# Kernel optimization log

Measured on AMD Instinct MI355X. Metric: run time of the kernel, lower is better.

Reference implementation:

```python
import jax, jax.numpy as jnp
import numpy as np

B, N, DIM = 4, 16384, 512
H, D, S = 8, 64, 64  # heads, dim_head, n_global_queries
SCALE = 1.0  # FLARE hardcodes scale=1.0


def setup_inputs() -> dict:
    key = jax.random.key(0)
    ks = jax.random.split(key, 10)
    inner = H * D
    s = 0.02
    return {
        "x": jax.random.normal(ks[0], (B, N, DIM), dtype=jnp.float32),
        "q_global": jax.random.normal(ks[1], (1, H, S, D), dtype=jnp.float32),
        "Wx": jax.random.normal(ks[2], (DIM, inner), dtype=jnp.float32) * s,
        "bx": jnp.zeros((inner,), dtype=jnp.float32),
        "Wk": jax.random.normal(ks[3], (D, D), dtype=jnp.float32) * s,
        "bk": jnp.zeros((D,), dtype=jnp.float32),
        "Wv": jax.random.normal(ks[4], (D, D), dtype=jnp.float32) * s,
        "bv": jnp.zeros((D,), dtype=jnp.float32),
        "Wo": jax.random.normal(ks[5], (inner, DIM), dtype=jnp.float32) * s,
        "bo": jnp.zeros((DIM,), dtype=jnp.float32),
    }


def reference(x, q_global, Wx, bx, Wk, bk, Wv, bv, Wo, bo):
    b, n, c = x.shape
    # input projection + split heads: B N (H D) -> B H N D
    x_mid = (x @ Wx + bx).reshape(b, n, H, D).transpose(0, 2, 1, 3)
    # per-head k/v projections (dim_head x dim_head)
    k = x_mid @ Wk + bk  # [B,H,N,D]
    v = x_mid @ Wv + bv  # [B,H,N,D]
    G = q_global  # broadcast over batch
    # pass 1: aggregate tokens into S global slots
    attn1 = jax.nn.softmax(jnp.einsum('bhsd,bhnd->bhsn', jnp.broadcast_to(G, (b, H, S, D)), k) * SCALE, axis=-1)
    z = jnp.einsum('bhsn,bhnd->bhsd', attn1, v)  # [B,H,S,D]
    # pass 2: distribute slots back to tokens (query=k, key=G, value=z)
    attn2 = jax.nn.softmax(jnp.einsum('bhnd,bhsd->bhns', k, jnp.broadcast_to(G, (b, H, S, D))) * SCALE, axis=-1)
    y = jnp.einsum('bhns,bhsd->bhnd', attn2, z)  # [B,H,N,D]
    # merge heads + output projection
    out = y.transpose(0, 2, 1, 3).reshape(b, n, H * D)
    return out @ Wo + bo
```

## Files before the change

### kernel.cpp

```cpp
#include <hip/hip_runtime.h>
#include <stdint.h>

#define DEV __device__ __forceinline__

typedef __attribute__((ext_vector_type(8))) short bf16x8;
typedef __attribute__((ext_vector_type(4))) float f32x4;
typedef __attribute__((ext_vector_type(8))) unsigned short u16x8;
typedef __attribute__((ext_vector_type(4))) unsigned short u16x4;

DEV unsigned short f2bf(float f) {
  union { float f; unsigned int u; } v; v.f = f;
  unsigned int u = v.u;
  return (unsigned short)((u + 0x7FFFu + ((u >> 16) & 1u)) >> 16);
}
DEV float bf2f(unsigned short u) {
  union { unsigned int u; float f; } v; v.u = ((unsigned int)u) << 16;
  return v.f;
}
DEV f32x4 mfma16(bf16x8 a, bf16x8 b, f32x4 c) {
  return __builtin_amdgcn_mfma_f32_16x16x32_bf16(a, b, c, 0, 0, 0);
}

__global__ __launch_bounds__(256) void k_cvt_bf16(const float* __restrict__ in,
                                                  unsigned short* __restrict__ out,
                                                  int n8) {
  int i = blockIdx.x * 256 + threadIdx.x;
  if (i >= n8) return;
  const float4* p = (const float4*)in + (size_t)i * 2;
  float4 a = p[0], b = p[1];
  u16x8 o;
  o[0] = f2bf(a.x); o[1] = f2bf(a.y); o[2] = f2bf(a.z); o[3] = f2bf(a.w);
  o[4] = f2bf(b.x); o[5] = f2bf(b.y); o[6] = f2bf(b.z); o[7] = f2bf(b.w);
  ((u16x8*)out)[i] = o;
}

__global__ void k_gk(const float* __restrict__ Wk, const float* __restrict__ qg,
                     float* __restrict__ GK) {
  int idx = blockIdx.x * 256 + threadIdx.x;
  int dd = idx & 63, hs = idx >> 6;
  float a = 0.f;
#pragma unroll 8
  for (int d = 0; d < 64; ++d) a += Wk[dd * 64 + d] * qg[(size_t)hs * 64 + d];
  GK[idx] = a;
}

__global__ void k_wl(const float* __restrict__ Wx, const float* __restrict__ GK,
                     unsigned short* __restrict__ Wcat) {
  int idx = blockIdx.x * 256 + threadIdx.x;
  int c = idx & 511, hs = idx >> 9;
  int h = hs >> 6;
  float a = 0.f;
#pragma unroll 8
  for (int dd = 0; dd < 64; ++dd) a += Wx[(size_t)c * 512 + h * 64 + dd] * GK[hs * 64 + dd];
  Wcat[(size_t)hs * 512 + c] = f2bf(a);
}

__global__ void k_wv(const float* __restrict__ Wx, const float* __restrict__ Wv,
                     unsigned short* __restrict__ Wcat) {
  int idx = blockIdx.x * 256 + threadIdx.x;
  int c = idx & 511, o = idx >> 9;
  int h = o >> 6, dp = o & 63;
  float a = 0.f;
#pragma unroll 8
  for (int dd = 0; dd < 64; ++dd) a += Wx[(size_t)c * 512 + h * 64 + dd] * Wv[dd * 64 + dp];
  Wcat[(size_t)(512 + o) * 512 + c] = f2bf(a);
}

__global__ void k_bias2(const float* __restrict__ bx, const float* __restrict__ bk,
                        const float* __restrict__ bv, const float* __restrict__ Wv,
                        const float* __restrict__ qg, const float* __restrict__ GK,
                        float* __restrict__ bias) {
  int o = blockIdx.x * 256 + threadIdx.x;
  if (o >= 1024) return;
  if (o < 512) {
    int h = o >> 6;
    float a = 0.f;
    for (int dd = 0; dd < 64; ++dd) a += bx[h * 64 + dd] * GK[(size_t)o * 64 + dd];
    for (int dp = 0; dp < 64; ++dp) a += bk[dp] * qg[(size_t)o * 64 + dp];
    bias[o] = a;
  } else {
    int o2 = o - 512, h = o2 >> 6, dp = o2 & 63;
    float a = bv[dp];
    for (int dd = 0; dd < 64; ++dd) a += bx[h * 64 + dd] * Wv[dd * 64 + dp];
    bias[o] = a;
  }
}

__global__ void k_wo_t(const float* __restrict__ Wo, unsigned short* __restrict__ WoT) {
  int idx = blockIdx.x * 256 + threadIdx.x;
  int i = idx >> 9, o = idx & 511;
  WoT[(size_t)o * 512 + i] = f2bf(Wo[(size_t)i * 512 + o]);
}

template <int MODE>
__global__ __launch_bounds__(512, 1) void k_mm2(const unsigned short* __restrict__ A,
                                                const unsigned short* __restrict__ Bsrc,
                                                const float* __restrict__ bias,
                                                unsigned short* __restrict__ P2,
                                                float* __restrict__ zpart,
                                                float* __restrict__ dpart,
                                                float* __restrict__ out) {
  extern __shared__ char lds[];
  const int tid = threadIdx.x, w = tid >> 6, lane = tid & 63, l = lane & 15, g = lane >> 4;
  unsigned bid = blockIdx.x;
  int mtile, h, ntile;
  if (MODE == 1) {
    int a = bid >> 3, c = bid & 7;
    mtile = (a & ~7) | c;
    h = a & 7;
    ntile = 0;
  } else {
    mtile = ((bid >> 5) << 3) | (bid & 7);
    ntile = (bid >> 3) & 3;
    h = 0;
  }
  const int bm = mtile * 256;
  const int b = bm >> 14;

  const unsigned short* Arow = A + (size_t)(bm + w * 32) * 512;
  bf16x8 af[16][2];
#pragma unroll
  for (int ks = 0; ks < 16; ++ks)
#pragma unroll
    for (int fm = 0; fm < 2; ++fm)
      af[ks][fm] = *(const bf16x8*)(Arow + (size_t)(fm * 16 + l) * 512 + ks * 32 + g * 8);

  {
    int col = tid >> 2;
    const unsigned short* src;
    if (MODE == 1)
      src = Bsrc + (size_t)((col < 64) ? h * 64 + col : 512 + h * 64 + (col - 64)) * 512;
    else
      src = Bsrc + ((size_t)b * 512 + ntile * 128 + col) * 512;
#pragma unroll
    for (int j = 0; j < 16; ++j) {
      int chunk = (tid & 3) + j * 4;
      u16x8 vv = *(const u16x8*)(src + chunk * 8);
      *(u16x8*)(lds + col * 1024 + ((chunk * 16) ^ ((col & 7) << 6))) = vv;
    }
  }
  __syncthreads();

  f32x4 acc[2][8] = {};
#pragma unroll
  for (int ks = 0; ks < 16; ++ks) {
    bf16x8 bfr[8];
#pragma unroll
    for (int fn = 0; fn < 8; ++fn)
      bfr[fn] = *(const bf16x8*)(lds + (fn * 16 + l) * 1024 + ((ks * 64 + g * 16) ^ ((l & 7) << 6)));
#pragma unroll
    for (int fn = 0; fn < 8; ++fn)
#pragma unroll
      for (int fm = 0; fm < 2; ++fm)
        acc[fm][fn] = mfma16(af[ks][fm], bfr[fn], acc[fm][fn]);
  }

  if (MODE == 0) {
    int nc0 = ntile * 128;
#pragma unroll
    for (int fm = 0; fm < 2; ++fm)
#pragma unroll
      for (int fn = 0; fn < 8; ++fn) {
        int colg = nc0 + fn * 16 + l;
        float bb = bias[colg];
#pragma unroll
        for (int r = 0; r < 4; ++r) {
          int row = bm + w * 32 + fm * 16 + g * 4 + r;
          out[(size_t)row * 512 + colg] = acc[fm][fn][r] + bb;
        }
      }
    return;
  }

  float be[4], bv4[4];
#pragma unroll
  for (int fn = 0; fn < 4; ++fn) be[fn] = bias[h * 64 + fn * 16 + l];
#pragma unroll
  for (int fn = 0; fn < 4; ++fn) bv4[fn] = bias[512 + h * 64 + fn * 16 + l];
#pragma unroll
  for (int fm = 0; fm < 2; ++fm) {
#pragma unroll
    for (int fn = 0; fn < 4; ++fn)
#pragma unroll
      for (int r = 0; r < 4; ++r)
        acc[fm][fn][r] = __expf(acc[fm][fn][r] + be[fn] - 8.0f);
#pragma unroll
    for (int fn = 4; fn < 8; ++fn)
#pragma unroll
      for (int r = 0; r < 4; ++r) acc[fm][fn][r] += bv4[fn - 4];
  }
  f32x4 rs[2];
#pragma unroll
  for (int fm = 0; fm < 2; ++fm)
#pragma unroll
    for (int r = 0; r < 4; ++r) {
      float t = (acc[fm][0][r] + acc[fm][1][r]) + (acc[fm][2][r] + acc[fm][3][r]);
#pragma unroll
      for (int m = 1; m < 16; m <<= 1) t += __shfl_xor(t, m);
      rs[fm][r] = t;
    }
  __syncthreads();
  unsigned short* ET = (unsigned short*)lds;
  unsigned short* VT = (unsigned short*)(lds + 33792);
  float* denp = (float*)(lds + 67584);
  int nb = w * 32;
#pragma unroll
  for (int fm = 0; fm < 2; ++fm)
#pragma unroll
    for (int fn = 0; fn < 4; ++fn)
#pragma unroll
      for (int r = 0; r < 4; ++r) {
        int nn = nb + fm * 16 + g * 4 + r;
        ET[(fn * 16 + l) * 264 + nn] = f2bf(acc[fm][fn][r]);
        VT[(fn * 16 + l) * 264 + nn] = f2bf(acc[fm][fn + 4][r]);
      }
#pragma unroll
  for (int fn = 0; fn < 4; ++fn) {
    float t = 0.f;
#pragma unroll
    for (int fm = 0; fm < 2; ++fm)
#pragma unroll
      for (int r = 0; r < 4; ++r) t += acc[fm][fn][r];
    t += __shfl_xor(t, 16);
    t += __shfl_xor(t, 32);
    if (g == 0) denp[w * 64 + fn * 16 + l] = t;
  }
#pragma unroll
  for (int fm = 0; fm < 2; ++fm)
#pragma unroll
    for (int r = 0; r < 4; ++r) {
      float rinv = 1.f / rs[fm][r];
      int nglob = bm + nb + fm * 16 + g * 4 + r;
#pragma unroll
      for (int fn = 0; fn < 4; ++fn)
        P2[(size_t)nglob * 512 + h * 64 + fn * 16 + l] = f2bf(acc[fm][fn][r] * rinv);
    }
  __syncthreads();
  size_t mh = (size_t)mtile * 8 + h;
  if (w < 4) {
    int s0 = w * 16;
    f32x4 za[4] = {};
#pragma unroll
    for (int ks2 = 0; ks2 < 8; ++ks2) {
      bf16x8 a2 = *(const bf16x8*)&ET[(s0 + l) * 264 + ks2 * 32 + g * 8];
#pragma unroll
      for (int fd = 0; fd < 4; ++fd) {
        bf16x8 b2 = *(const bf16x8*)&VT[(fd * 16 + l) * 264 + ks2 * 32 + g * 8];
        za[fd] = mfma16(a2, b2, za[fd]);
      }
    }
#pragma unroll
    for (int fd = 0; fd < 4; ++fd)
#pragma unroll
      for (int r = 0; r < 4; ++r)
        zpart[mh * 4096 + (s0 + g * 4 + r) * 64 + fd * 16 + l] = za[fd][r];
  } else if (w == 4) {
    int s = lane;
    float t = 0.f;
#pragma unroll
    for (int ww = 0; ww < 8; ++ww) t += denp[ww * 64 + s];
    dpart[mh * 64 + s] = t;
  }
}

__global__ void k_zred(const float* __restrict__ zpart, const float* __restrict__ dpart,
                       float* __restrict__ z) {
  int idx = blockIdx.x * 256 + threadIdx.x;
  int bh = idx >> 12, s = (idx >> 6) & 63, d = idx & 63;
  int b = bh >> 3, h = bh & 7;
  float num = 0.f, den = 0.f;
  for (int mm = 0; mm < 64; ++mm) {
    size_t mh = ((size_t)(b * 64 + mm)) * 8 + h;
    num += zpart[mh * 4096 + s * 64 + d];
    den += dpart[mh * 64 + s];
  }
  z[idx] = num / den;
}

__global__ void k_zwo(const float* __restrict__ z, const unsigned short* __restrict__ WoT,
                      unsigned short* __restrict__ zWoT) {
  int idx = blockIdx.x * 256 + threadIdx.x;
  int hs = idx & 511, c = (idx >> 9) & 511, b = idx >> 18;
  int h = hs >> 6;
  const float* zp = z + ((size_t)(b * 8 + h) * 64 + (hs & 63)) * 64;
  const unsigned short* wp = WoT + (size_t)c * 512 + h * 64;
  float a = 0.f;
#pragma unroll 8
  for (int d = 0; d < 64; ++d) a += zp[d] * bf2f(wp[d]);
  zWoT[((size_t)(b * 512) + c) * 512 + hs] = f2bf(a);
}

extern "C" void kernel_launch(void* const* d_in, const int* in_sizes, int n_in,
                              void* d_out, int out_size, void* d_ws, size_t ws_size,
                              hipStream_t stream) {
  const float* x  = (const float*)d_in[0];
  const float* qg = (const float*)d_in[1];
  const float* Wx = (const float*)d_in[2];
  const float* bx = (const float*)d_in[3];
  const float* Wk = (const float*)d_in[4];
  const float* bk = (const float*)d_in[5];
  const float* Wv = (const float*)d_in[6];
  const float* bv = (const float*)d_in[7];
  const float* Wo = (const float*)d_in[8];
  const float* bo = (const float*)d_in[9];
  float* out = (float*)d_out;

  char* ws = (char*)d_ws;
  unsigned short* xbf  = (unsigned short*)(ws);
  unsigned short* P2   = (unsigned short*)(ws + 67108864);
  unsigned short* Wcat = (unsigned short*)(ws + 134217728);
  unsigned short* WoT  = (unsigned short*)(ws + 135266304);
  float* bias          = (float*)(ws + 135790592);
  float* GK            = (float*)(ws + 135794688);
  unsigned short* zWoT = (unsigned short*)(ws + 135925760);
  float* zbuf          = (float*)(ws + 138027008);
  char* dob = (char*)d_out;
  float* zpart = (float*)(dob);
  float* dpart = (float*)(dob + 33554432);

  k_cvt_bf16<<<dim3(16384), dim3(256), 0, stream>>>(x, xbf, 4194304);
  k_gk<<<dim3(128), dim3(256), 0, stream>>>(Wk, qg, GK);
  k_wl<<<dim3(1024), dim3(256), 0, stream>>>(Wx, GK, Wcat);
  k_wv<<<dim3(1024), dim3(256), 0, stream>>>(Wx, Wv, Wcat);
  k_bias2<<<dim3(4), dim3(256), 0, stream>>>(bx, bk, bv, Wv, qg, GK, bias);
  k_wo_t<<<dim3(1024), dim3(256), 0, stream>>>(Wo, WoT);
  k_mm2<1><<<dim3(2048), dim3(512), 131072, stream>>>(xbf, Wcat, bias, P2, zpart, dpart,
                                                      nullptr);
  k_zred<<<dim3(512), dim3(256), 0, stream>>>(zpart, dpart, zbuf);
  k_zwo<<<dim3(4096), dim3(256), 0, stream>>>(zbuf, WoT, zWoT);
  k_mm2<0><<<dim3(1024), dim3(512), 131072, stream>>>(P2, zWoT, bo, nullptr, nullptr,
                                                      nullptr, out);
}
```

Measured before the change: 326.2 us.

## Retile both GEMMs to 128x128 K-looped tiles with direct global-to-LDS loads

Replaces the 256-row, 512-thread, full-K-in-registers GEMM kernel with a 128x128 tile, 256-thread kernel that walks K in 64-wide steps, staging A and B through swizzled LDS with global_load_lds. Wcat is re-laid out so each head's logit and value columns sit in one contiguous 128-column block, and the epilogue splits exp/normalise and value-bias work across warp pairs. The goal is a smaller LDS footprint and fewer registers so four blocks fit per CU, giving better occupancy and latency hiding. In exchange the loop has no double buffering, there are twice as many z partials for k_zred to reduce, and the dpart offset moves.

```diff
diff --git a/kernel.cpp b/kernel.cpp
--- a/kernel.cpp
+++ b/kernel.cpp
@@ -6,7 +6,6 @@
 typedef __attribute__((ext_vector_type(8))) short bf16x8;
 typedef __attribute__((ext_vector_type(4))) float f32x4;
 typedef __attribute__((ext_vector_type(8))) unsigned short u16x8;
-typedef __attribute__((ext_vector_type(4))) unsigned short u16x4;
 
 DEV unsigned short f2bf(float f) {
   union { float f; unsigned int u; } v; v.f = f;
@@ -19,6 +18,11 @@
 }
 DEV f32x4 mfma16(bf16x8 a, bf16x8 b, f32x4 c) {
   return __builtin_amdgcn_mfma_f32_16x16x32_bf16(a, b, c, 0, 0, 0);
+}
+DEV void gl_lds16(const void* g, void* l) {
+  __builtin_amdgcn_global_load_lds(
+      (const __attribute__((address_space(1))) void*)g,
+      (__attribute__((address_space(3))) void*)l, 16, 0, 0);
 }
 
 __global__ __launch_bounds__(256) void k_cvt_bf16(const float* __restrict__ in,
@@ -48,11 +52,11 @@
                      unsigned short* __restrict__ Wcat) {
   int idx = blockIdx.x * 256 + threadIdx.x;
   int c = idx & 511, hs = idx >> 9;
-  int h = hs >> 6;
+  int h = hs >> 6, s = hs & 63;
   float a = 0.f;
 #pragma unroll 8
   for (int dd = 0; dd < 64; ++dd) a += Wx[(size_t)c * 512 + h * 64 + dd] * GK[hs * 64 + dd];
-  Wcat[(size_t)hs * 512 + c] = f2bf(a);
+  Wcat[(size_t)(h * 128 + s) * 512 + c] = f2bf(a);
 }
 
 __global__ void k_wv(const float* __restrict__ Wx, const float* __restrict__ Wv,
@@ -63,7 +67,7 @@
   float a = 0.f;
 #pragma unroll 8
   for (int dd = 0; dd < 64; ++dd) a += Wx[(size_t)c * 512 + h * 64 + dd] * Wv[dd * 64 + dp];
-  Wcat[(size_t)(512 + o) * 512 + c] = f2bf(a);
+  Wcat[(size_t)(h * 128 + 64 + dp) * 512 + c] = f2bf(a);
 }
 
 __global__ void k_bias2(const float* __restrict__ bx, const float* __restrict__ bk,
@@ -72,14 +76,15 @@
                         float* __restrict__ bias) {
   int o = blockIdx.x * 256 + threadIdx.x;
   if (o >= 1024) return;
-  if (o < 512) {
-    int h = o >> 6;
+  int h = o >> 7, j = o & 127;
+  if (j < 64) {
+    int hs = h * 64 + j;
     float a = 0.f;
-    for (int dd = 0; dd < 64; ++dd) a += bx[h * 64 + dd] * GK[(size_t)o * 64 + dd];
-    for (int dp = 0; dp < 64; ++dp) a += bk[dp] * qg[(size_t)o * 64 + dp];
+    for (int dd = 0; dd < 64; ++dd) a += bx[h * 64 + dd] * GK[(size_t)hs * 64 + dd];
+    for (int dp = 0; dp < 64; ++dp) a += bk[dp] * qg[(size_t)hs * 64 + dp];
     bias[o] = a;
   } else {
-    int o2 = o - 512, h = o2 >> 6, dp = o2 & 63;
+    int dp = j - 64;
     float a = bv[dp];
     for (int dd = 0; dd < 64; ++dd) a += bx[h * 64 + dd] * Wv[dd * 64 + dp];
     bias[o] = a;
@@ -93,174 +98,160 @@
 }
 
 template <int MODE>
-__global__ __launch_bounds__(512, 1) void k_mm2(const unsigned short* __restrict__ A,
-                                                const unsigned short* __restrict__ Bsrc,
-                                                const float* __restrict__ bias,
-                                                unsigned short* __restrict__ P2,
-                                                float* __restrict__ zpart,
-                                                float* __restrict__ dpart,
-                                                float* __restrict__ out) {
-  extern __shared__ char lds[];
-  const int tid = threadIdx.x, w = tid >> 6, lane = tid & 63, l = lane & 15, g = lane >> 4;
+__global__ __launch_bounds__(256, 4) void k_mm(const unsigned short* __restrict__ A,
+                                               const unsigned short* __restrict__ BTg,
+                                               const float* __restrict__ bias,
+                                               unsigned short* __restrict__ P2,
+                                               float* __restrict__ zpart,
+                                               float* __restrict__ dpart,
+                                               float* __restrict__ outF) {
+  __shared__ __align__(16) char lds[35328];
+  const int tid = threadIdx.x;
+  const int w = tid >> 6, lane = tid & 63, l = lane & 15, g = lane >> 4;
   unsigned bid = blockIdx.x;
-  int mtile, h, ntile;
+  int mtile, ntile;
   if (MODE == 1) {
-    int a = bid >> 3, c = bid & 7;
-    mtile = (a & ~7) | c;
-    h = a & 7;
-    ntile = 0;
+    unsigned nbid = (bid & 7) * 512 + (bid >> 3);
+    mtile = nbid >> 3;
+    ntile = nbid & 7;
   } else {
-    mtile = ((bid >> 5) << 3) | (bid & 7);
-    ntile = (bid >> 3) & 3;
-    h = 0;
-  }
-  const int bm = mtile * 256;
-  const int b = bm >> 14;
-
-  const unsigned short* Arow = A + (size_t)(bm + w * 32) * 512;
-  bf16x8 af[16][2];
-#pragma unroll
-  for (int ks = 0; ks < 16; ++ks)
-#pragma unroll
-    for (int fm = 0; fm < 2; ++fm)
-      af[ks][fm] = *(const bf16x8*)(Arow + (size_t)(fm * 16 + l) * 512 + ks * 32 + g * 8);
-
-  {
-    int col = tid >> 2;
-    const unsigned short* src;
-    if (MODE == 1)
-      src = Bsrc + (size_t)((col < 64) ? h * 64 + col : 512 + h * 64 + (col - 64)) * 512;
-    else
-      src = Bsrc + ((size_t)b * 512 + ntile * 128 + col) * 512;
-#pragma unroll
-    for (int j = 0; j < 16; ++j) {
-      int chunk = (tid & 3) + j * 4;
-      u16x8 vv = *(const u16x8*)(src + chunk * 8);
-      *(u16x8*)(lds + col * 1024 + ((chunk * 16) ^ ((col & 7) << 6))) = vv;
-    }
-  }
-  __syncthreads();
-
-  f32x4 acc[2][8] = {};
-#pragma unroll
-  for (int ks = 0; ks < 16; ++ks) {
-    bf16x8 bfr[8];
-#pragma unroll
-    for (int fn = 0; fn < 8; ++fn)
-      bfr[fn] = *(const bf16x8*)(lds + (fn * 16 + l) * 1024 + ((ks * 64 + g * 16) ^ ((l & 7) << 6)));
-#pragma unroll
-    for (int fn = 0; fn < 8; ++fn)
-#pragma unroll
-      for (int fm = 0; fm < 2; ++fm)
-        acc[fm][fn] = mfma16(af[ks][fm], bfr[fn], acc[fm][fn]);
+    unsigned nbid = (bid & 7) * 256 + (bid >> 3);
+    mtile = nbid >> 2;
+    ntile = nbid & 3;
+  }
+  const int bm = mtile * 128;
+  const int bn = ntile * 128;
+  const int b = mtile >> 7;
+  const unsigned short* BT = (MODE == 0) ? BTg + ((size_t)b << 18) : BTg;
+  const int wm = (w >> 1) * 64, wn = (w & 1) * 64;
+  char* As = lds;
+  char* Bs = lds + 16384;
+  f32x4 acc[4][4] = {};
+  const int sw = (l & 7) << 4;
+
+  for (int t = 0; t < 8; ++t) {
+#pragma unroll
+    for (int i = 0; i < 4; ++i) {
+      int off = i * 4096 + tid * 16;
+      int row = off >> 7;
+      int cb = (off & 127) ^ ((row & 7) << 4);
+      gl_lds16(A + (size_t)(bm + row) * 512 + t * 64 + (cb >> 1), As + off);
+      gl_lds16(BT + (size_t)(bn + row) * 512 + t * 64 + (cb >> 1), Bs + off);
+    }
+    __syncthreads();
+#pragma unroll
+    for (int ks = 0; ks < 2; ++ks) {
+      int kb = (ks * 64 + g * 16) ^ sw;
+      bf16x8 af[4], bf[4];
+#pragma unroll
+      for (int fm = 0; fm < 4; ++fm)
+        af[fm] = *(const bf16x8*)(As + (wm + fm * 16 + l) * 128 + kb);
+#pragma unroll
+      for (int fn = 0; fn < 4; ++fn)
+        bf[fn] = *(const bf16x8*)(Bs + (wn + fn * 16 + l) * 128 + kb);
+#pragma unroll
+      for (int fm = 0; fm < 4; ++fm)
+#pragma unroll
+        for (int fn = 0; fn < 4; ++fn)
+          acc[fm][fn] = mfma16(af[fm], bf[fn], acc[fm][fn]);
+    }
+    __syncthreads();
   }
 
   if (MODE == 0) {
-    int nc0 = ntile * 128;
-#pragma unroll
-    for (int fm = 0; fm < 2; ++fm)
-#pragma unroll
-      for (int fn = 0; fn < 8; ++fn) {
-        int colg = nc0 + fn * 16 + l;
-        float bb = bias[colg];
-#pragma unroll
-        for (int r = 0; r < 4; ++r) {
-          int row = bm + w * 32 + fm * 16 + g * 4 + r;
-          out[(size_t)row * 512 + colg] = acc[fm][fn][r] + bb;
-        }
+#pragma unroll
+    for (int fm = 0; fm < 4; ++fm)
+#pragma unroll
+      for (int fn = 0; fn < 4; ++fn) {
+        int col = bn + wn + fn * 16 + l;
+        float bb = bias[col];
+#pragma unroll
+        for (int r = 0; r < 4; ++r)
+          outF[(size_t)(bm + wm + fm * 16 + g * 4 + r) * 512 + col] = acc[fm][fn][r] + bb;
       }
     return;
   }
 
-  float be[4], bv4[4];
-#pragma unroll
-  for (int fn = 0; fn < 4; ++fn) be[fn] = bias[h * 64 + fn * 16 + l];
-#pragma unroll
-  for (int fn = 0; fn < 4; ++fn) bv4[fn] = bias[512 + h * 64 + fn * 16 + l];
-#pragma unroll
-  for (int fm = 0; fm < 2; ++fm) {
-#pragma unroll
-    for (int fn = 0; fn < 4; ++fn)
-#pragma unroll
-      for (int r = 0; r < 4; ++r)
-        acc[fm][fn][r] = __expf(acc[fm][fn][r] + be[fn] - 8.0f);
-#pragma unroll
-    for (int fn = 4; fn < 8; ++fn)
-#pragma unroll
-      for (int r = 0; r < 4; ++r) acc[fm][fn][r] += bv4[fn - 4];
-  }
-  f32x4 rs[2];
-#pragma unroll
-  for (int fm = 0; fm < 2; ++fm)
-#pragma unroll
-    for (int r = 0; r < 4; ++r) {
-      float t = (acc[fm][0][r] + acc[fm][1][r]) + (acc[fm][2][r] + acc[fm][3][r]);
-#pragma unroll
-      for (int m = 1; m < 16; m <<= 1) t += __shfl_xor(t, m);
-      rs[fm][r] = t;
-    }
+  const int h = ntile;
+  unsigned short* ET = (unsigned short*)lds;
+  unsigned short* VT = (unsigned short*)(lds + 17408);
+  float* denp = (float*)(lds + 34816);
+  float bc[4];
+#pragma unroll
+  for (int fn = 0; fn < 4; ++fn) bc[fn] = bias[h * 128 + wn + fn * 16 + l];
+  if (wn == 0) {
+#pragma unroll
+    for (int fm = 0; fm < 4; ++fm)
+#pragma unroll
+      for (int fn = 0; fn < 4; ++fn)
+#pragma unroll
+        for (int r = 0; r < 4; ++r)
+          acc[fm][fn][r] = __expf(acc[fm][fn][r] + bc[fn] - 8.0f);
+#pragma unroll
+    for (int fm = 0; fm < 4; ++fm) {
+      f32x4 rs;
+#pragma unroll
+      for (int r = 0; r < 4; ++r) {
+        float t2 = (acc[fm][0][r] + acc[fm][1][r]) + (acc[fm][2][r] + acc[fm][3][r]);
+#pragma unroll
+        for (int m = 1; m < 16; m <<= 1) t2 += __shfl_xor(t2, m);
+        rs[r] = t2;
+      }
+#pragma unroll
+      for (int r = 0; r < 4; ++r) {
+        float rinv = 1.f / rs[r];
+        int n = bm + wm + fm * 16 + g * 4 + r;
+#pragma unroll
+        for (int fn = 0; fn < 4; ++fn)
+          P2[(size_t)n * 512 + h * 64 + fn * 16 + l] = f2bf(acc[fm][fn][r] * rinv);
+      }
+    }
+#pragma unroll
+    for (int fm = 0; fm < 4; ++fm)
+#pragma unroll
+      for (int fn = 0; fn < 4; ++fn)
+#pragma unroll
+        for (int r = 0; r < 4; ++r)
+          ET[(fn * 16 + l) * 136 + wm + fm * 16 + g * 4 + r] = f2bf(acc[fm][fn][r]);
+#pragma unroll
+    for (int fn = 0; fn < 4; ++fn) {
+      float t2 = 0.f;
+#pragma unroll
+      for (int fm = 0; fm < 4; ++fm)
+#pragma unroll
+        for (int r = 0; r < 4; ++r) t2 += acc[fm][fn][r];
+      t2 += __shfl_xor(t2, 16);
+      t2 += __shfl_xor(t2, 32);
+      if (g == 0) denp[(w >> 1) * 64 + fn * 16 + l] = t2;
+    }
+  } else {
+#pragma unroll
+    for (int fm = 0; fm < 4; ++fm)
+#pragma unroll
+      for (int fn = 0; fn < 4; ++fn)
+#pragma unroll
+        for (int r = 0; r < 4; ++r)
+          VT[(fn * 16 + l) * 136 + wm + fm * 16 + g * 4 + r] =
+              f2bf(acc[fm][fn][r] + bc[fn]);
+  }
   __syncthreads();
-  unsigned short* ET = (unsigned short*)lds;
-  unsigned short* VT = (unsigned short*)(lds + 33792);
-  float* denp = (float*)(lds + 67584);
-  int nb = w * 32;
-#pragma unroll
-  for (int fm = 0; fm < 2; ++fm)
-#pragma unroll
-    for (int fn = 0; fn < 4; ++fn)
-#pragma unroll
-      for (int r = 0; r < 4; ++r) {
-        int nn = nb + fm * 16 + g * 4 + r;
-        ET[(fn * 16 + l) * 264 + nn] = f2bf(acc[fm][fn][r]);
-        VT[(fn * 16 + l) * 264 + nn] = f2bf(acc[fm][fn + 4][r]);
-      }
-#pragma unroll
-  for (int fn = 0; fn < 4; ++fn) {
-    float t = 0.f;
-#pragma unroll
-    for (int fm = 0; fm < 2; ++fm)
-#pragma unroll
-      for (int r = 0; r < 4; ++r) t += acc[fm][fn][r];
-    t += __shfl_xor(t, 16);
-    t += __shfl_xor(t, 32);
-    if (g == 0) denp[w * 64 + fn * 16 + l] = t;
-  }
-#pragma unroll
-  for (int fm = 0; fm < 2; ++fm)
-#pragma unroll
-    for (int r = 0; r < 4; ++r) {
-      float rinv = 1.f / rs[fm][r];
-      int nglob = bm + nb + fm * 16 + g * 4 + r;
-#pragma unroll
-      for (int fn = 0; fn < 4; ++fn)
-        P2[(size_t)nglob * 512 + h * 64 + fn * 16 + l] = f2bf(acc[fm][fn][r] * rinv);
-    }
-  __syncthreads();
+  f32x4 za[4] = {};
+#pragma unroll
+  for (int ks2 = 0; ks2 < 4; ++ks2) {
+    bf16x8 a2 = *(const bf16x8*)&ET[(w * 16 + l) * 136 + ks2 * 32 + g * 8];
+#pragma unroll
+    for (int fd = 0; fd < 4; ++fd) {
+      bf16x8 b2 = *(const bf16x8*)&VT[(fd * 16 + l) * 136 + ks2 * 32 + g * 8];
+      za[fd] = mfma16(a2, b2, za[fd]);
+    }
+  }
   size_t mh = (size_t)mtile * 8 + h;
-  if (w < 4) {
-    int s0 = w * 16;
-    f32x4 za[4] = {};
-#pragma unroll
-    for (int ks2 = 0; ks2 < 8; ++ks2) {
-      bf16x8 a2 = *(const bf16x8*)&ET[(s0 + l) * 264 + ks2 * 32 + g * 8];
-#pragma unroll
-      for (int fd = 0; fd < 4; ++fd) {
-        bf16x8 b2 = *(const bf16x8*)&VT[(fd * 16 + l) * 264 + ks2 * 32 + g * 8];
-        za[fd] = mfma16(a2, b2, za[fd]);
-      }
-    }
-#pragma unroll
-    for (int fd = 0; fd < 4; ++fd)
-#pragma unroll
-      for (int r = 0; r < 4; ++r)
-        zpart[mh * 4096 + (s0 + g * 4 + r) * 64 + fd * 16 + l] = za[fd][r];
-  } else if (w == 4) {
-    int s = lane;
-    float t = 0.f;
-#pragma unroll
-    for (int ww = 0; ww < 8; ++ww) t += denp[ww * 64 + s];
-    dpart[mh * 64 + s] = t;
-  }
+#pragma unroll
+  for (int fd = 0; fd < 4; ++fd)
+#pragma unroll
+    for (int r = 0; r < 4; ++r)
+      zpart[mh * 4096 + (w * 16 + g * 4 + r) * 64 + fd * 16 + l] = za[fd][r];
+  if (w == 0) dpart[mh * 64 + lane] = denp[lane] + denp[64 + lane];
 }
 
 __global__ void k_zred(const float* __restrict__ zpart, const float* __restrict__ dpart,
@@ -269,8 +260,8 @@
   int bh = idx >> 12, s = (idx >> 6) & 63, d = idx & 63;
   int b = bh >> 3, h = bh & 7;
   float num = 0.f, den = 0.f;
-  for (int mm = 0; mm < 64; ++mm) {
-    size_t mh = ((size_t)(b * 64 + mm)) * 8 + h;
+  for (int mm = 0; mm < 128; ++mm) {
+    size_t mh = ((size_t)(b * 128 + mm)) * 8 + h;
     num += zpart[mh * 4096 + s * 64 + d];
     den += dpart[mh * 64 + s];
   }
@@ -316,7 +307,7 @@
   float* zbuf          = (float*)(ws + 138027008);
   char* dob = (char*)d_out;
   float* zpart = (float*)(dob);
-  float* dpart = (float*)(dob + 33554432);
+  float* dpart = (float*)(dob + 67108864);
 
   k_cvt_bf16<<<dim3(16384), dim3(256), 0, stream>>>(x, xbf, 4194304);
   k_gk<<<dim3(128), dim3(256), 0, stream>>>(Wk, qg, GK);
@@ -324,10 +315,8 @@
   k_wv<<<dim3(1024), dim3(256), 0, stream>>>(Wx, Wv, Wcat);
   k_bias2<<<dim3(4), dim3(256), 0, stream>>>(bx, bk, bv, Wv, qg, GK, bias);
   k_wo_t<<<dim3(1024), dim3(256), 0, stream>>>(Wo, WoT);
-  k_mm2<1><<<dim3(2048), dim3(512), 131072, stream>>>(xbf, Wcat, bias, P2, zpart, dpart,
-                                                      nullptr);
+  k_mm<1><<<dim3(4096), dim3(256), 0, stream>>>(xbf, Wcat, bias, P2, zpart, dpart, nullptr);
   k_zred<<<dim3(512), dim3(256), 0, stream>>>(zpart, dpart, zbuf);
   k_zwo<<<dim3(4096), dim3(256), 0, stream>>>(zbuf, WoT, zWoT);
-  k_mm2<0><<<dim3(1024), dim3(512), 131072, stream>>>(P2, zWoT, bo, nullptr, nullptr,
-                                                      nullptr, out);
-}
+  k_mm<0><<<dim3(2048), dim3(256), 0, stream>>>(P2, zWoT, bo, nullptr, nullptr, nullptr, out);
+}
```

New measurement: 284.1 us. -12.9%, faster.
